# Optimization experiments

Measured on AMD Instinct MI355X. Metric: run time of the kernel, lower is better.

Reference implementation:

```python
import jax, jax.numpy as jnp
import numpy as np

N, IN_F, OUT_F, K = 256, 8192, 8320, 16
J = OUT_F - IN_F  # 128


def setup_inputs() -> dict:
    key = jax.random.key(0)
    k1, k2 = jax.random.split(key)
    tensor = jax.random.normal(k1, (N, IN_F), dtype=jnp.float32)
    T = jax.random.normal(k2, (IN_F, J, K), dtype=jnp.float32)
    return {"tensor": tensor, "T": T}


def reference(tensor, T):
    # flatten(start_dim=1) is identity for rank-2 input
    x = tensor.reshape(tensor.shape[0], -1)            # [N, IN_F]
    feats = jnp.einsum('ni,ijk->njk', x, T)            # [N, J, K]
    # pairwise L1 across batch: [N,1,J,K] - [N,J,K] -> [N,N,J,K]
    diff = jnp.abs(feats[:, None, :, :] - feats[None, :, :, :])
    l1 = jnp.sum(diff, axis=3)                         # [N, N, J]
    diversity = jnp.sum(jnp.exp(-l1), axis=1)          # [N, J]
    return jnp.concatenate((x, diversity), axis=1)     # [N, IN_F + J]
```

## Files before the change

### kernel.cpp

```cpp
#include <hip/hip_runtime.h>

typedef unsigned int  u32;
typedef unsigned short u16;

typedef __bf16 bf16x8 __attribute__((ext_vector_type(8)));
typedef float  floatx4 __attribute__((ext_vector_type(4)));

#define N_ROWS 256
#define IN_F   8192
#define OUT_F  8320
#define JDIM   128
#define KDIM   16
#define JK     2048

#define BN      64
#define KSLAB   512
#define NSLAB   16
#define WSTRIDE 520

__device__ __forceinline__ u16 f2bf(float f) {
    u32 u = __float_as_uint(f);
    return (u16)((u + 0x7fffu + ((u >> 16) & 1u)) >> 16);
}
__device__ __forceinline__ float bf2f(u16 h) { return __uint_as_float(((u32)h) << 16); }

__global__ __launch_bounds__(256) void prep_kernel(const float* __restrict__ X,
                                                   float* __restrict__ out,
                                                   u16* __restrict__ Xb)
{
    int t = blockIdx.x * 256 + threadIdx.x;
    float4 v = reinterpret_cast<const float4*>(X)[t];
    int row = t >> 11;
    int c4  = t & 2047;
    reinterpret_cast<float4*>(out + (size_t)row * OUT_F)[c4] = v;
    ushort4 b;
    b.x = f2bf(v.x); b.y = f2bf(v.y); b.z = f2bf(v.z); b.w = f2bf(v.w);
    reinterpret_cast<ushort4*>(Xb)[t] = b;
    if (t < 8192) {
        int r2 = t >> 5, j4 = t & 31;
        reinterpret_cast<float4*>(out + (size_t)r2 * OUT_F + IN_F)[j4] = make_float4(0.f, 0.f, 0.f, 0.f);
    }
}

__global__ __launch_bounds__(256) void gemm_kernel(const u16* __restrict__ Xb,
                                                   const float* __restrict__ W,
                                                   u16* __restrict__ slabs)
{
    __shared__ u16 wt[BN * WSTRIDE];

    const int tid  = threadIdx.x;
    const int lane = tid & 63;
    const int wave = tid >> 6;
    const int c0   = blockIdx.x * BN;
    const int s    = blockIdx.y;
    const int k0   = s * KSLAB;

    {
        const int wc4 = (tid & 15) << 2;
        const int wk4 = (tid >> 4) << 2;
        const float* wp0 = W + (size_t)(k0 + wk4) * JK + c0 + wc4;

        float4 wr[2][4];
        #pragma unroll
        for (int r = 0; r < 4; ++r) wr[0][r] = *(const float4*)(wp0 + (size_t)r * JK);
        #pragma unroll
        for (int r = 0; r < 4; ++r) wr[1][r] = *(const float4*)(wp0 + (size_t)(64 + r) * JK);

        #pragma unroll
        for (int p = 0; p < 8; ++p) {
            float4* cur = wr[p & 1];
            u32 pk[4][2];
            #pragma unroll
            for (int i = 0; i < 4; ++i) {
                const float* c = (const float*)cur;
                pk[i][0] = (u32)f2bf(c[0 * 4 + i]) | ((u32)f2bf(c[1 * 4 + i]) << 16);
                pk[i][1] = (u32)f2bf(c[2 * 4 + i]) | ((u32)f2bf(c[3 * 4 + i]) << 16);
            }
            if (p + 2 < 8) {
                const float* wn = wp0 + (size_t)(p + 2) * 64 * JK;
                #pragma unroll
                for (int r = 0; r < 4; ++r) cur[r] = *(const float4*)(wn + (size_t)r * JK);
            }
            #pragma unroll
            for (int i = 0; i < 4; ++i)
                *(uint2*)&wt[(wc4 + i) * WSTRIDE + p * 64 + wk4] = *(uint2*)pk[i];
        }
    }
    __syncthreads();

    const int mrow = lane & 15;
    const int q    = lane >> 4;

    floatx4 acc[4][4] = {};

    const u16* arow[4];
    #pragma unroll
    for (int rt = 0; rt < 4; ++rt)
        arow[rt] = Xb + (size_t)(wave * 64 + rt * 16 + mrow) * IN_F + k0 + q * 8;

    bf16x8 a[4], an[4];
    #pragma unroll
    for (int rt = 0; rt < 4; ++rt) a[rt] = *(const bf16x8*)(arow[rt]);

    for (int kc = 0; kc < 16; ++kc) {
        if (kc + 1 < 16) {
            #pragma unroll
            for (int rt = 0; rt < 4; ++rt)
                an[rt] = *(const bf16x8*)(arow[rt] + (kc + 1) * 32);
        }
        bf16x8 b[4];
        #pragma unroll
        for (int ct = 0; ct < 4; ++ct) {
            int col = ct * 16 + mrow;
            b[ct] = *(const bf16x8*)(&wt[col * WSTRIDE + kc * 32 + q * 8]);
        }
        #pragma unroll
        for (int rt = 0; rt < 4; ++rt)
            #pragma unroll
            for (int ct = 0; ct < 4; ++ct)
                acc[rt][ct] = __builtin_amdgcn_mfma_f32_16x16x32_bf16(a[rt], b[ct], acc[rt][ct], 0, 0, 0);
        #pragma unroll
        for (int rt = 0; rt < 4; ++rt) a[rt] = an[rt];
    }

    const int qe = lane >> 4;
    const int cl = lane & 15;
    u16* sp = slabs + (size_t)s * N_ROWS * JK;
    #pragma unroll
    for (int rt = 0; rt < 4; ++rt)
        #pragma unroll
        for (int ct = 0; ct < 4; ++ct)
            #pragma unroll
            for (int r = 0; r < 4; ++r) {
                int row = wave * 64 + rt * 16 + qe * 4 + r;
                int col = c0 + ct * 16 + cl;
                sp[(size_t)row * JK + col] = f2bf(acc[rt][ct][r]);
            }
}

__global__ __launch_bounds__(256) void reduce_kernel(const u16* __restrict__ slabs,
                                                     float* __restrict__ feats)
{
    int t = blockIdx.x * 256 + threadIdx.x;
    float acc[8] = {};
    for (int s = 0; s < NSLAB; ++s) {
        uint4 v = *(const uint4*)(slabs + (size_t)s * N_ROWS * JK + (size_t)t * 8);
        const u16* h = (const u16*)&v;
        #pragma unroll
        for (int e = 0; e < 8; ++e) acc[e] += bf2f(h[e]);
    }
    float4* fp = (float4*)(feats + (size_t)t * 8);
    fp[0] = make_float4(acc[0], acc[1], acc[2], acc[3]);
    fp[1] = make_float4(acc[4], acc[5], acc[6], acc[7]);
}

__global__ __launch_bounds__(256) void pairwise_kernel(const float* __restrict__ feats,
                                                       float* __restrict__ out)
{
    const int j = blockIdx.x;
    const int mq = blockIdx.y;
    const int n = threadIdx.x;

    __shared__ float F[N_ROWS * KDIM];
    const float* fr = feats + (size_t)n * JK + j * KDIM;
    float4 v0 = ((const float4*)fr)[0];
    float4 v1 = ((const float4*)fr)[1];
    float4 v2 = ((const float4*)fr)[2];
    float4 v3 = ((const float4*)fr)[3];
    float4* Fp = (float4*)&F[n * KDIM];
    Fp[0] = v0; Fp[1] = v1; Fp[2] = v2; Fp[3] = v3;
    __syncthreads();

    float f[16] = { v0.x, v0.y, v0.z, v0.w, v1.x, v1.y, v1.z, v1.w,
                    v2.x, v2.y, v2.z, v2.w, v3.x, v3.y, v3.z, v3.w };
    float accum = 0.f;
    const int m0 = mq * 64;
    for (int m = 0; m < 64; ++m) {
        const float* Fm = &F[(m0 + m) * KDIM];
        float l1 = 0.f;
        #pragma unroll
        for (int k = 0; k < 16; ++k) l1 += fabsf(f[k] - Fm[k]);
        accum += exp2f(-1.4426950408889634f * l1);
    }
    atomicAdd(&out[(size_t)n * OUT_F + IN_F + j], accum);
}

extern "C" void kernel_launch(void* const* d_in, const int* in_sizes, int n_in,
                              void* d_out, int out_size, void* d_ws, size_t ws_size,
                              hipStream_t stream)
{
    const float* X = (const float*)d_in[0];
    const float* T = (const float*)d_in[1];
    float* out = (float*)d_out;

    float* feats = (float*)d_ws;
    u16*   Xb    = (u16*)((char*)d_ws + (2u << 20));
    u16*   slabs = (u16*)((char*)d_ws + (6u << 20));

    prep_kernel<<<2048, 256, 0, stream>>>(X, out, Xb);
    gemm_kernel<<<dim3(JK / BN, NSLAB), 256, 0, stream>>>(Xb, T, slabs);
    reduce_kernel<<<256, 256, 0, stream>>>(slabs, feats);
    pairwise_kernel<<<dim3(JDIM, 4), 256, 0, stream>>>(feats, out);
}
```

Measured before the change: 143.5 us.

## Halve GEMM K-slab, double split-K slabs, swizzle LDS weight tile

```diff
diff --git a/kernel.cpp b/kernel.cpp
--- a/kernel.cpp
+++ b/kernel.cpp
@@ -14,9 +14,8 @@
 #define JK     2048
 
 #define BN      64
-#define KSLAB   512
-#define NSLAB   16
-#define WSTRIDE 520
+#define KSLAB   256
+#define NSLAB   32
 
 __device__ __forceinline__ u16 f2bf(float f) {
     u32 u = __float_as_uint(f);
@@ -42,11 +41,11 @@
     }
 }
 
-__global__ __launch_bounds__(256) void gemm_kernel(const u16* __restrict__ Xb,
-                                                   const float* __restrict__ W,
-                                                   u16* __restrict__ slabs)
+__global__ __launch_bounds__(256, 3) void gemm_kernel(const u16* __restrict__ Xb,
+                                                      const float* __restrict__ W,
+                                                      u16* __restrict__ slabs)
 {
-    __shared__ u16 wt[BN * WSTRIDE];
+    __shared__ u16 wt[BN * KSLAB];
 
     const int tid  = threadIdx.x;
     const int lane = tid & 63;
@@ -56,34 +55,28 @@
     const int k0   = s * KSLAB;
 
     {
-        const int wc4 = (tid & 15) << 2;
-        const int wk4 = (tid >> 4) << 2;
-        const float* wp0 = W + (size_t)(k0 + wk4) * JK + c0 + wc4;
-
-        float4 wr[2][4];
+        const float* wbase = W + (size_t)(k0 + wave * 64) * JK + c0 + lane;
+        float v[4][8];
         #pragma unroll
-        for (int r = 0; r < 4; ++r) wr[0][r] = *(const float4*)(wp0 + (size_t)r * JK);
-        #pragma unroll
-        for (int r = 0; r < 4; ++r) wr[1][r] = *(const float4*)(wp0 + (size_t)(64 + r) * JK);
+        for (int ch = 0; ch < 4; ++ch)
+            #pragma unroll
+            for (int r = 0; r < 8; ++r)
+                v[ch][r] = wbase[(size_t)(ch * 8 + r) * JK];
 
         #pragma unroll
-        for (int p = 0; p < 8; ++p) {
-            float4* cur = wr[p & 1];
-            u32 pk[4][2];
+        for (int ch = 0; ch < 8; ++ch) {
+            u32 pk[4];
             #pragma unroll
-            for (int i = 0; i < 4; ++i) {
-                const float* c = (const float*)cur;
-                pk[i][0] = (u32)f2bf(c[0 * 4 + i]) | ((u32)f2bf(c[1 * 4 + i]) << 16);
-                pk[i][1] = (u32)f2bf(c[2 * 4 + i]) | ((u32)f2bf(c[3 * 4 + i]) << 16);
+            for (int j = 0; j < 4; ++j)
+                pk[j] = (u32)f2bf(v[ch & 3][2 * j]) | ((u32)f2bf(v[ch & 3][2 * j + 1]) << 16);
+            if (ch + 4 < 8) {
+                #pragma unroll
+                for (int r = 0; r < 8; ++r)
+                    v[ch & 3][r] = wbase[(size_t)((ch + 4) * 8 + r) * JK];
             }
-            if (p + 2 < 8) {
-                const float* wn = wp0 + (size_t)(p + 2) * 64 * JK;
-                #pragma unroll
-                for (int r = 0; r < 4; ++r) cur[r] = *(const float4*)(wn + (size_t)r * JK);
-            }
-            #pragma unroll
-            for (int i = 0; i < 4; ++i)
-                *(uint2*)&wt[(wc4 + i) * WSTRIDE + p * 64 + wk4] = *(uint2*)pk[i];
+            int gch  = wave * 8 + ch;
+            int slot = gch ^ (lane & 7);
+            *(uint4*)&wt[lane * KSLAB + slot * 8] = *(uint4*)pk;
         }
     }
     __syncthreads();
@@ -102,8 +95,8 @@
     #pragma unroll
     for (int rt = 0; rt < 4; ++rt) a[rt] = *(const bf16x8*)(arow[rt]);
 
-    for (int kc = 0; kc < 16; ++kc) {
-        if (kc + 1 < 16) {
+    for (int kc = 0; kc < 8; ++kc) {
+        if (kc + 1 < 8) {
             #pragma unroll
             for (int rt = 0; rt < 4; ++rt)
                 an[rt] = *(const bf16x8*)(arow[rt] + (kc + 1) * 32);
@@ -111,8 +104,10 @@
         bf16x8 b[4];
         #pragma unroll
         for (int ct = 0; ct < 4; ++ct) {
-            int col = ct * 16 + mrow;
-            b[ct] = *(const bf16x8*)(&wt[col * WSTRIDE + kc * 32 + q * 8]);
+            int col   = ct * 16 + mrow;
+            int chunk = kc * 4 + q;
+            int slot  = chunk ^ (col & 7);
+            b[ct] = *(const bf16x8*)(&wt[col * KSLAB + slot * 8]);
         }
         #pragma unroll
         for (int rt = 0; rt < 4; ++rt)
```

After: 153.0 us. 1.07x slower.

## Load W directly into MFMA B registers, dropping the LDS staging of weights

Applied to the files above, without the earlier changes.

```diff
diff --git a/kernel.cpp b/kernel.cpp
--- a/kernel.cpp
+++ b/kernel.cpp
@@ -4,6 +4,7 @@
 typedef unsigned short u16;
 
 typedef __bf16 bf16x8 __attribute__((ext_vector_type(8)));
+typedef u32    u32x4  __attribute__((ext_vector_type(4)));
 typedef float  floatx4 __attribute__((ext_vector_type(4)));
 
 #define N_ROWS 256
@@ -16,7 +17,6 @@
 #define BN      64
 #define KSLAB   512
 #define NSLAB   16
-#define WSTRIDE 520
 
 __device__ __forceinline__ u16 f2bf(float f) {
     u32 u = __float_as_uint(f);
@@ -46,8 +46,6 @@
                                                    const float* __restrict__ W,
                                                    u16* __restrict__ slabs)
 {
-    __shared__ u16 wt[BN * WSTRIDE];
-
     const int tid  = threadIdx.x;
     const int lane = tid & 63;
     const int wave = tid >> 6;
@@ -55,86 +53,78 @@
     const int s    = blockIdx.y;
     const int k0   = s * KSLAB;
 
-    {
-        const int wc4 = (tid & 15) << 2;
-        const int wk4 = (tid >> 4) << 2;
-        const float* wp0 = W + (size_t)(k0 + wk4) * JK + c0 + wc4;
+    const int h  = wave >> 1;
+    const int cc = wave & 1;
+    const int n  = lane & 15;
+    const int q  = lane >> 4;
 
-        float4 wr[2][4];
+    floatx4 acc[8][2] = {};
+
+    const u32* wbase = (const u32*)W + (size_t)(k0 + q * 8) * JK + c0 + cc * 32 + n;
+    const u16* abase = Xb + k0 + q * 8;
+
+    u32 ub[2][8], ubn[2][8];
+    bf16x8 a[8], an[8];
+
+    #pragma unroll
+    for (int cbi = 0; cbi < 2; ++cbi)
         #pragma unroll
-        for (int r = 0; r < 4; ++r) wr[0][r] = *(const float4*)(wp0 + (size_t)r * JK);
+        for (int j = 0; j < 8; ++j)
+            ub[cbi][j] = wbase[(size_t)j * JK + cbi * 16];
+    #pragma unroll
+    for (int rf = 0; rf < 8; ++rf)
+        a[rf] = *(const bf16x8*)(abase + (size_t)(h * 128 + rf * 16 + n) * IN_F);
+
+    const int KC = KSLAB / 32;
+    for (int kc = 0; kc < KC; ++kc) {
+        if (kc + 1 < KC) {
+            const u32* wp = wbase + (size_t)(kc + 1) * 32 * JK;
+            #pragma unroll
+            for (int cbi = 0; cbi < 2; ++cbi)
+                #pragma unroll
+                for (int j = 0; j < 8; ++j)
+                    ubn[cbi][j] = wp[(size_t)j * JK + cbi * 16];
+            #pragma unroll
+            for (int rf = 0; rf < 8; ++rf)
+                an[rf] = *(const bf16x8*)(abase + (size_t)(h * 128 + rf * 16 + n) * IN_F + (kc + 1) * 32);
+        }
+
+        bf16x8 b[2];
         #pragma unroll
-        for (int r = 0; r < 4; ++r) wr[1][r] = *(const float4*)(wp0 + (size_t)(64 + r) * JK);
+        for (int cbi = 0; cbi < 2; ++cbi) {
+            u32x4 pk;
+            #pragma unroll
+            for (int t = 0; t < 4; ++t)
+                pk[t] = (ub[cbi][2 * t] >> 16) | (ub[cbi][2 * t + 1] & 0xffff0000u);
+            b[cbi] = __builtin_bit_cast(bf16x8, pk);
+        }
 
         #pragma unroll
-        for (int p = 0; p < 8; ++p) {
-            float4* cur = wr[p & 1];
-            u32 pk[4][2];
+        for (int rf = 0; rf < 8; ++rf)
             #pragma unroll
-            for (int i = 0; i < 4; ++i) {
-                const float* c = (const float*)cur;
-                pk[i][0] = (u32)f2bf(c[0 * 4 + i]) | ((u32)f2bf(c[1 * 4 + i]) << 16);
-                pk[i][1] = (u32)f2bf(c[2 * 4 + i]) | ((u32)f2bf(c[3 * 4 + i]) << 16);
-            }
-            if (p + 2 < 8) {
-                const float* wn = wp0 + (size_t)(p + 2) * 64 * JK;
-                #pragma unroll
-                for (int r = 0; r < 4; ++r) cur[r] = *(const float4*)(wn + (size_t)r * JK);
-            }
+            for (int cbi = 0; cbi < 2; ++cbi)
+                acc[rf][cbi] = __builtin_amdgcn_mfma_f32_16x16x32_bf16(a[rf], b[cbi], acc[rf][cbi], 0, 0, 0);
+
+        #pragma unroll
+        for (int cbi = 0; cbi < 2; ++cbi)
             #pragma unroll
-            for (int i = 0; i < 4; ++i)
-                *(uint2*)&wt[(wc4 + i) * WSTRIDE + p * 64 + wk4] = *(uint2*)pk[i];
-        }
-    }
-    __syncthreads();
-
-    const int mrow = lane & 15;
-    const int q    = lane >> 4;
-
-    floatx4 acc[4][4] = {};
-
-    const u16* arow[4];
-    #pragma unroll
-    for (int rt = 0; rt < 4; ++rt)
-        arow[rt] = Xb + (size_t)(wave * 64 + rt * 16 + mrow) * IN_F + k0 + q * 8;
-
-    bf16x8 a[4], an[4];
-    #pragma unroll
-    for (int rt = 0; rt < 4; ++rt) a[rt] = *(const bf16x8*)(arow[rt]);
-
-    for (int kc = 0; kc < 16; ++kc) {
-        if (kc + 1 < 16) {
-            #pragma unroll
-            for (int rt = 0; rt < 4; ++rt)
-                an[rt] = *(const bf16x8*)(arow[rt] + (kc + 1) * 32);
-        }
-        bf16x8 b[4];
+            for (int j = 0; j < 8; ++j)
+                ub[cbi][j] = ubn[cbi][j];
         #pragma unroll
-        for (int ct = 0; ct < 4; ++ct) {
-            int col = ct * 16 + mrow;
-            b[ct] = *(const bf16x8*)(&wt[col * WSTRIDE + kc * 32 + q * 8]);
-        }
-        #pragma unroll
-        for (int rt = 0; rt < 4; ++rt)
-            #pragma unroll
-            for (int ct = 0; ct < 4; ++ct)
-                acc[rt][ct] = __builtin_amdgcn_mfma_f32_16x16x32_bf16(a[rt], b[ct], acc[rt][ct], 0, 0, 0);
-        #pragma unroll
-        for (int rt = 0; rt < 4; ++rt) a[rt] = an[rt];
+        for (int rf = 0; rf < 8; ++rf)
+            a[rf] = an[rf];
     }
 
-    const int qe = lane >> 4;
-    const int cl = lane & 15;
     u16* sp = slabs + (size_t)s * N_ROWS * JK;
     #pragma unroll
-    for (int rt = 0; rt < 4; ++rt)
+    for (int rf = 0; rf < 8; ++rf)
         #pragma unroll
-        for (int ct = 0; ct < 4; ++ct)
+        for (int cbi = 0; cbi < 2; ++cbi)
             #pragma unroll
             for (int r = 0; r < 4; ++r) {
-                int row = wave * 64 + rt * 16 + qe * 4 + r;
-                int col = c0 + ct * 16 + cl;
-                sp[(size_t)row * JK + col] = f2bf(acc[rt][ct][r]);
+                int row = h * 128 + rf * 16 + q * 4 + r;
+                int col = c0 + cc * 32 + cbi * 16 + n;
+                sp[(size_t)row * JK + col] = f2bf(acc[rf][cbi][r]);
             }
 }
 
```

Measured after the change: 158.7 us. 1.11x slower.
